# Kernel optimization log

Hardware: AMD Instinct MI355X
Metric: run time of the kernel (lower is better)

The kernel has to match this reference:

```python
import jax, jax.numpy as jnp
import numpy as np

B, T, I, H, FUT = 16384, 50, 6, 128, 30


def setup_inputs() -> dict:
    key = jax.random.key(0)
    ks = jax.random.split(key, 10)
    bound = 1.0 / np.sqrt(H)
    u = lambda k, shape: jax.random.uniform(k, shape, jnp.float32, -bound, bound)
    return {
        "history": jax.random.normal(ks[0], (B, T, I), jnp.float32),
        # GRU weights (PyTorch layout: gates stacked [r, z, n])
        "w_ih": u(ks[1], (3 * H, I)),
        "w_hh": u(ks[2], (3 * H, H)),
        "b_ih": u(ks[3], (3 * H,)),
        "b_hh": u(ks[4], (3 * H,)),
        # MLP head: Linear(H,H) -> ReLU -> Linear(H,I)
        "w1": u(ks[5], (H, H)),
        "b1": u(ks[6], (H,)),
        "w2": u(ks[7], (I, H)),
        "b2": u(ks[8], (I,)),
    }


def _gru_cell(h, x, w_ih, w_hh, b_ih, b_hh):
    # PyTorch GRU cell: gates ordered r, z, n
    gi = x @ w_ih.T + b_ih          # (B, 3H)
    gh = h @ w_hh.T + b_hh          # (B, 3H)
    i_r, i_z, i_n = jnp.split(gi, 3, axis=-1)
    h_r, h_z, h_n = jnp.split(gh, 3, axis=-1)
    r = jax.nn.sigmoid(i_r + h_r)
    z = jax.nn.sigmoid(i_z + h_z)
    n = jnp.tanh(i_n + r * h_n)
    return (1.0 - z) * n + z * h


def reference(history, w_ih, w_hh, b_ih, b_hh, w1, b1, w2, b2):
    # --- encode history: scan GRU over time ---
    h0 = jnp.zeros((history.shape[0], H), history.dtype)

    def enc_step(h, x_t):
        return _gru_cell(h, x_t, w_ih, w_hh, b_ih, b_hh), None

    h_last, _ = jax.lax.scan(enc_step, h0, jnp.swapaxes(history, 0, 1))  # (B, H)

    def head(h):
        return jax.nn.relu(h @ w1.T + b1) @ w2.T + b2  # (B, I)

    def dec_step(carry, _):
        h, x = carry
        h = _gru_cell(h, x, w_ih, w_hh, b_ih, b_hh)
        x = head(h)
        return (h, x), x

    x0 = history[:, -1]  # (B, I)
    _, preds = jax.lax.scan(dec_step, (h_last, x0), None, length=FUT)  # (FUT, B, I)
    return jnp.swapaxes(preds, 0, 1)  # (B, FUT, I)
```

## Files before the change

kernel.cpp:

```cpp
#include <hip/hip_runtime.h>

typedef _Float16 half8 __attribute__((ext_vector_type(8)));
typedef _Float16 half4 __attribute__((ext_vector_type(4)));
typedef float f32x4 __attribute__((ext_vector_type(4)));
typedef int int4v __attribute__((ext_vector_type(4)));

#define ROWS 32
#define NC (ROWS / 16)
#define HP 136
#define HBUFSZ (ROWS * HP)
#define LOG2E 1.442695041f
#define MFMA(a,b,c) __builtin_amdgcn_mfma_f32_16x16x32_f16((a),(b),(c),0,0,0)

__global__ __launch_bounds__(512, 2)
void traj_gru(const float* __restrict__ history,
              const float* __restrict__ w_ih, const float* __restrict__ w_hh,
              const float* __restrict__ b_ih, const float* __restrict__ b_hh,
              const float* __restrict__ w1, const float* __restrict__ b1,
              const float* __restrict__ w2, const float* __restrict__ b2,
              float* __restrict__ out)
{
    __shared__ __align__(16) _Float16 hbuf[2 * HBUFSZ];
    __shared__ __align__(16) _Float16 xhist[50 * ROWS * 6];
    __shared__ __align__(16) _Float16 xdec[ROWS * 8];
    __shared__ __align__(16) _Float16 w2f[4 * 4 * 16 * 8];

    const int tid  = threadIdx.x;
    const int wave = tid >> 6;
    const int lane = tid & 63;
    const int ln16 = lane & 15;
    const int q    = lane >> 4;
    const int sw   = ln16 & 3;
    const int rowbase = blockIdx.x * ROWS;
    const int dbase = wave * 16;
    const int bblk  = wave >> 1;
    const int colin = ((wave & 1) << 4) | ln16;

    for (int i = tid; i < 2 * HBUFSZ; i += 512) hbuf[i] = (_Float16)0;
    for (int i = tid; i < ROWS * 8; i += 512) xdec[i] = (_Float16)0;
    for (int i = tid; i < 4 * 4 * 16 * 8; i += 512) w2f[i] = (_Float16)0;
    __syncthreads();
    for (int idx = tid; idx < ROWS * 300; idx += 512) {
        int r = idx / 300, rem = idx - r * 300;
        int t = rem / 6, c = rem - t * 6;
        xhist[(t * ROWS + r) * 6 + c] = (_Float16)history[(rowbase + r) * 300 + rem];
    }
    if (tid < ROWS) xdec[tid * 8 + 6] = (_Float16)1.0f;
    for (int idx = tid; idx < 6 * 128; idx += 512) {
        int n = idx >> 7, k = idx & 127;
        int kt = k >> 5, qq = (k >> 3) & 3, j = k & 7;
        w2f[((kt * 4 + qq) * 16 + n) * 8 + j] = (_Float16)w2[n * 128 + k];
    }

    half8 Wg[3][4];
    #pragma unroll
    for (int g = 0; g < 3; ++g) {
        float sc = (g < 2) ? -LOG2E : -2.0f * LOG2E;
        #pragma unroll
        for (int kt = 0; kt < 4; ++kt) {
            const float* p = w_hh + (g * 128 + dbase + ln16) * 128 + kt * 32 + q * 8;
            half8 v;
            #pragma unroll
            for (int j = 0; j < 8; ++j) v[j] = (_Float16)(p[j] * sc);
            Wg[g][kt] = v;
        }
    }
    half8 Wx[3];
    #pragma unroll
    for (int g = 0; g < 3; ++g) {
        float sc = (g < 2) ? -LOG2E : -2.0f * LOG2E;
        half8 v;
        #pragma unroll
        for (int j = 0; j < 8; ++j) v[j] = (_Float16)0.0f;
        if (q == 0) {
            #pragma unroll
            for (int j = 0; j < 6; ++j) v[j] = (_Float16)(w_ih[(g * 128 + dbase + ln16) * 6 + j] * sc);
        }
        Wx[g] = v;
    }
    f32x4 brr, brz, bin, bhn;
    #pragma unroll
    for (int i = 0; i < 4; ++i) {
        int d = dbase + q * 4 + i;
        brr[i] = (b_ih[d]       + b_hh[d]      ) * (-LOG2E);
        brz[i] = (b_ih[128 + d] + b_hh[128 + d]) * (-LOG2E);
        bin[i] = b_ih[256 + d] * (-2.0f * LOG2E);
        bhn[i] = b_hh[256 + d] * (-2.0f * LOG2E);
    }
    half8 Bw1[4];
    #pragma unroll
    for (int kt = 0; kt < 4; ++kt) {
        const float* p = w1 + (dbase + ln16) * 128 + kt * 32 + q * 8;
        half8 v;
        #pragma unroll
        for (int j = 0; j < 8; ++j) v[j] = (_Float16)p[j];
        Bw1[kt] = v;
    }
    const float b1r = b1[dbase + ln16];
    const float b2r = (ln16 < 6) ? b2[ln16] : 0.0f;

    float hp[NC][4] = {};

    __syncthreads();

    auto gru_step = [&](int p, int t, bool enc) {
        const _Float16* hb = hbuf + p * HBUFSZ;
        _Float16*       hn = hbuf + (p ^ 1) * HBUFSZ;
        half8 Bf[2][4], Bx[2];
        f32x4 ar[2], az[2], ahh[2], an[2];

        auto loadB = [&](int c, int buf) {
            const _Float16* rp = hb + (c * 16 + ln16) * HP;
            #pragma unroll
            for (int kt = 0; kt < 4; ++kt)
                Bf[buf][kt] = *(const half8*)(rp + kt * 32 + q * 8);
            if (enc) {
                const int* xi = (const int*)xhist;
                int base = (t * ROWS + c * 16 + ln16) * 3;
                int4v d = { xi[base], xi[base + 1], xi[base + 2], 0x3C00 };
                Bx[buf] = __builtin_bit_cast(half8, d);
            } else {
                Bx[buf] = *(const half8*)(xdec + (c * 16 + ln16) * 8);
            }
        };
        auto mfmas = [&](int buf) {
            f32x4 r = brr, z = brz, hh = bhn, n = bin;
            #pragma unroll
            for (int kt = 0; kt < 4; ++kt) {
                r  = MFMA(Wg[0][kt], Bf[buf][kt], r);
                z  = MFMA(Wg[1][kt], Bf[buf][kt], z);
                hh = MFMA(Wg[2][kt], Bf[buf][kt], hh);
            }
            r = MFMA(Wx[0], Bx[buf], r);
            z = MFMA(Wx[1], Bx[buf], z);
            n = MFMA(Wx[2], Bx[buf], n);
            ar[buf] = r; az[buf] = z; ahh[buf] = hh; an[buf] = n;
        };
        auto gates = [&](int c, int cb) {
            half4 hv;
            #pragma unroll
            for (int i = 0; i < 4; ++i) {
                float r = __builtin_amdgcn_rcpf(1.0f + __builtin_amdgcn_exp2f(ar[cb][i]));
                float z = __builtin_amdgcn_rcpf(1.0f + __builtin_amdgcn_exp2f(az[cb][i]));
                float tt = an[cb][i] + r * ahh[cb][i];
                float n = 2.0f * __builtin_amdgcn_rcpf(1.0f + __builtin_amdgcn_exp2f(tt)) - 1.0f;
                float h = n + z * (hp[c][i] - n);
                hp[c][i] = h;
                hv[i] = (_Float16)h;
            }
            *(half4*)(hn + (c * 16 + ln16) * HP + dbase + q * 4) = hv;
        };

        loadB(0, 0); mfmas(0);
        #pragma unroll
        for (int c = 0; c < NC; ++c) {
            const int cb = c & 1;
            if (c < NC - 1) { loadB(c + 1, cb ^ 1); mfmas(cb ^ 1); }
            gates(c, cb);
        }
        __syncthreads();
    };

    auto head_step = [&](int f, int p) {
        const _Float16* hb = hbuf + p * HBUFSZ;
        _Float16*       a1 = hbuf + (p ^ 1) * HBUFSZ;
        half8 Ah[2][4];
        f32x4 aa[2];
        auto loadA = [&](int c, int buf) {
            const _Float16* rp = hb + (c * 16 + ln16) * HP;
            #pragma unroll
            for (int kt = 0; kt < 4; ++kt)
                Ah[buf][kt] = *(const half8*)(rp + kt * 32 + q * 8);
        };
        auto mfh = [&](int buf) {
            f32x4 a = {0,0,0,0};
            #pragma unroll
            for (int kt = 0; kt < 4; ++kt) a = MFMA(Ah[buf][kt], Bw1[kt], a);
            aa[buf] = a;
        };
        auto relu4 = [&](int c, int cb) {
            #pragma unroll
            for (int i = 0; i < 4; ++i) {
                float v = aa[cb][i] + b1r;
                v = v > 0.0f ? v : 0.0f;
                a1[(c * 16 + q * 4 + i) * HP + ((bblk ^ i) << 5) + colin] = (_Float16)v;
            }
        };
        loadA(0, 0); mfh(0);
        #pragma unroll
        for (int c = 0; c < NC; ++c) {
            const int cb = c & 1;
            if (c < NC - 1) { loadA(c + 1, cb ^ 1); mfh(cb ^ 1); }
            relu4(c, cb);
        }
        __syncthreads();
        if (wave < NC) {
            const _Float16* rp = a1 + (wave * 16 + ln16) * HP;
            f32x4 o = {0,0,0,0};
            #pragma unroll
            for (int kt = 0; kt < 4; ++kt) {
                half8 Aa = *(const half8*)(rp + ((kt ^ sw) << 5) + q * 8);
                half8 Bw = *(const half8*)&w2f[((kt * 4 + q) * 16 + ln16) * 8];
                o = MFMA(Aa, Bw, o);
            }
            if (ln16 < 6) {
                #pragma unroll
                for (int i = 0; i < 4; ++i) {
                    int row = wave * 16 + q * 4 + i;
                    float v = o[i] + b2r;
                    out[(rowbase + row) * 180 + f * 6 + ln16] = v;
                    xdec[row * 8 + ln16] = (_Float16)v;
                }
            }
        }
        __syncthreads();
    };

    int p = 0;
    #pragma unroll 1
    for (int t = 0; t < 50; ++t) { gru_step(p, t, true); p ^= 1; }
    #pragma unroll 1
    for (int f = 0; f < 30; ++f) {
        gru_step(p, f == 0 ? 49 : 0, f == 0);
        p ^= 1;
        head_step(f, p);
    }
}

extern "C" void kernel_launch(void* const* d_in, const int* in_sizes, int n_in,
                              void* d_out, int out_size, void* d_ws, size_t ws_size,
                              hipStream_t stream) {
    (void)in_sizes; (void)n_in; (void)d_ws; (void)ws_size; (void)out_size;
    traj_gru<<<dim3(16384 / ROWS), dim3(512), 0, stream>>>(
        (const float*)d_in[0], (const float*)d_in[1], (const float*)d_in[2],
        (const float*)d_in[3], (const float*)d_in[4], (const float*)d_in[5],
        (const float*)d_in[6], (const float*)d_in[7], (const float*)d_in[8],
        (float*)d_out);
}
```

Measured before the change: 294.7 us.

## Move W1 and input weights to LDS to cut registers for higher occupancy

Moves the MLP first-layer weights and the GRU input weights out of per-thread registers into shared memory, reloading them from LDS inside the MFMA loops. The launch hint changes from two blocks per CU to four waves per EU, so the compiler has to fit fewer registers per thread and more waves can run to hide latency. In exchange every step issues extra LDS reads, and shared memory grows by about 38 KB per block, which may limit how many blocks fit on a CU.

```diff
diff --git a/kernel.cpp b/kernel.cpp
--- a/kernel.cpp
+++ b/kernel.cpp
@@ -12,7 +12,7 @@
 #define LOG2E 1.442695041f
 #define MFMA(a,b,c) __builtin_amdgcn_mfma_f32_16x16x32_f16((a),(b),(c),0,0,0)
 
-__global__ __launch_bounds__(512, 2)
+__global__ __launch_bounds__(512) __attribute__((amdgpu_waves_per_eu(4)))
 void traj_gru(const float* __restrict__ history,
               const float* __restrict__ w_ih, const float* __restrict__ w_hh,
               const float* __restrict__ b_ih, const float* __restrict__ b_hh,
@@ -24,6 +24,8 @@
     __shared__ __align__(16) _Float16 xhist[50 * ROWS * 6];
     __shared__ __align__(16) _Float16 xdec[ROWS * 8];
     __shared__ __align__(16) _Float16 w2f[4 * 4 * 16 * 8];
+    __shared__ __align__(16) _Float16 w1f[4 * 4 * 128 * 8];
+    __shared__ __align__(16) _Float16 wxf[3 * 128 * 8];
 
     const int tid  = threadIdx.x;
     const int wave = tid >> 6;
@@ -51,6 +53,17 @@
         int kt = k >> 5, qq = (k >> 3) & 3, j = k & 7;
         w2f[((kt * 4 + qq) * 16 + n) * 8 + j] = (_Float16)w2[n * 128 + k];
     }
+    for (int idx = tid; idx < 128 * 128; idx += 512) {
+        int d = idx >> 7, k = idx & 127;
+        int kt = k >> 5, qq = (k >> 3) & 3, j = k & 7;
+        w1f[((kt * 4 + qq) * 128 + d) * 8 + j] = (_Float16)w1[idx];
+    }
+    for (int idx = tid; idx < 3 * 128 * 8; idx += 512) {
+        int j = idx & 7, gd = idx >> 3;
+        int g = gd >> 7;
+        float sc = (g < 2) ? -LOG2E : -2.0f * LOG2E;
+        wxf[idx] = (j < 6) ? (_Float16)(w_ih[gd * 6 + j] * sc) : (_Float16)0.0f;
+    }
 
     half8 Wg[3][4];
     #pragma unroll
@@ -65,19 +78,6 @@
             Wg[g][kt] = v;
         }
     }
-    half8 Wx[3];
-    #pragma unroll
-    for (int g = 0; g < 3; ++g) {
-        float sc = (g < 2) ? -LOG2E : -2.0f * LOG2E;
-        half8 v;
-        #pragma unroll
-        for (int j = 0; j < 8; ++j) v[j] = (_Float16)0.0f;
-        if (q == 0) {
-            #pragma unroll
-            for (int j = 0; j < 6; ++j) v[j] = (_Float16)(w_ih[(g * 128 + dbase + ln16) * 6 + j] * sc);
-        }
-        Wx[g] = v;
-    }
     f32x4 brr, brz, bin, bhn;
     #pragma unroll
     for (int i = 0; i < 4; ++i) {
@@ -86,15 +86,6 @@
         brz[i] = (b_ih[128 + d] + b_hh[128 + d]) * (-LOG2E);
         bin[i] = b_ih[256 + d] * (-2.0f * LOG2E);
         bhn[i] = b_hh[256 + d] * (-2.0f * LOG2E);
-    }
-    half8 Bw1[4];
-    #pragma unroll
-    for (int kt = 0; kt < 4; ++kt) {
-        const float* p = w1 + (dbase + ln16) * 128 + kt * 32 + q * 8;
-        half8 v;
-        #pragma unroll
-        for (int j = 0; j < 8; ++j) v[j] = (_Float16)p[j];
-        Bw1[kt] = v;
     }
     const float b1r = b1[dbase + ln16];
     const float b2r = (ln16 < 6) ? b2[ln16] : 0.0f;
@@ -131,9 +122,16 @@
                 z  = MFMA(Wg[1][kt], Bf[buf][kt], z);
                 hh = MFMA(Wg[2][kt], Bf[buf][kt], hh);
             }
-            r = MFMA(Wx[0], Bx[buf], r);
-            z = MFMA(Wx[1], Bx[buf], z);
-            n = MFMA(Wx[2], Bx[buf], n);
+            const half8 zero8 = {};
+            half8 wx0 = *(const half8*)(wxf + ((0 * 128 + dbase + ln16) << 3));
+            half8 wx1 = *(const half8*)(wxf + ((1 * 128 + dbase + ln16) << 3));
+            half8 wx2 = *(const half8*)(wxf + ((2 * 128 + dbase + ln16) << 3));
+            wx0 = (q == 0) ? wx0 : zero8;
+            wx1 = (q == 0) ? wx1 : zero8;
+            wx2 = (q == 0) ? wx2 : zero8;
+            r = MFMA(wx0, Bx[buf], r);
+            z = MFMA(wx1, Bx[buf], z);
+            n = MFMA(wx2, Bx[buf], n);
             ar[buf] = r; az[buf] = z; ahh[buf] = hh; an[buf] = n;
         };
         auto gates = [&](int c, int cb) {
@@ -175,7 +173,10 @@
         auto mfh = [&](int buf) {
             f32x4 a = {0,0,0,0};
             #pragma unroll
-            for (int kt = 0; kt < 4; ++kt) a = MFMA(Ah[buf][kt], Bw1[kt], a);
+            for (int kt = 0; kt < 4; ++kt) {
+                half8 bw = *(const half8*)(w1f + (((kt * 4 + q) * 128) + dbase + ln16) * 8);
+                a = MFMA(Ah[buf][kt], bw, a);
+            }
             aa[buf] = a;
         };
         auto relu4 = [&](int c, int cb) {
```

After: 454.8 us. +54.3%, slower.
